# Performance work log

Hardware: AMD Instinct MI355X
Metric: run time of the kernel (lower is better)

The kernel has to match this reference:

```python
import jax, jax.numpy as jnp
import numpy as np

B, SD, VD, AD, E, K = 32768, 96, 512, 12, 8, 2
EPS_LN = 1e-5

def _ln(x, g, b):
    m = x.mean(-1, keepdims=True)
    v = ((x - m) ** 2).mean(-1, keepdims=True)
    return (x - m) / jnp.sqrt(v + EPS_LN) * g + b

def setup_inputs() -> dict:
    key = jax.random.key(0)
    ks = iter(jax.random.split(key, 64))
    def w(shape, s=0.02):
        return jax.random.normal(next(ks), shape, dtype=jnp.float32) * s
    inp = {
        'state_obs': jax.random.normal(next(ks), (B, SD), dtype=jnp.float32),
        'vlm_feature': jax.random.normal(next(ks), (B, VD), dtype=jnp.float32),
        # state encoder (per-expert stacked): 96->256->128, Linear+ELU+LN each
        'sw1': w((E, SD, 256)), 'sb1': jnp.zeros((E, 256)), 'sg1': jnp.ones((E, 256)), 'sh1': jnp.zeros((E, 256)),
        'sw2': w((E, 256, 128)), 'sb2': jnp.zeros((E, 128)), 'sg2': jnp.ones((E, 128)), 'sh2': jnp.zeros((E, 128)),
        # vlm encoder: 512->512->256
        'vw1': w((E, VD, 512)), 'vb1': jnp.zeros((E, 512)), 'vg1': jnp.ones((E, 512)), 'vh1': jnp.zeros((E, 512)),
        'vw2': w((E, 512, 256)), 'vb2': jnp.zeros((E, 256)), 'vg2': jnp.ones((E, 256)), 'vh2': jnp.zeros((E, 256)),
        # fusion: (128+256)=384 -> 512 -> 256 -> 12 (act+LN except last)
        'fw1': w((E, 384, 512)), 'fb1': jnp.zeros((E, 512)), 'fg1': jnp.ones((E, 512)), 'fh1': jnp.zeros((E, 512)),
        'fw2': w((E, 512, 256)), 'fb2': jnp.zeros((E, 256)), 'fg2': jnp.ones((E, 256)), 'fh2': jnp.zeros((E, 256)),
        'fw3': w((E, 256, AD)), 'fb3': jnp.zeros((E, AD)),
        # gate: (96+512)=608 -> 256 -> 128 -> 8, act between hidden layers only
        'gw1': w((SD + VD, 256)), 'gb1': jnp.zeros((256,)),
        'gw2': w((256, 128)), 'gb2': jnp.zeros((128,)),
        'gw3': w((128, E)), 'gb3': jnp.zeros((E,)),
        'logstd': jnp.full((AD,), -1.0, dtype=jnp.float32),
    }
    return inp

def reference(state_obs, vlm_feature,
              sw1, sb1, sg1, sh1, sw2, sb2, sg2, sh2,
              vw1, vb1, vg1, vh1, vw2, vb2, vg2, vh2,
              fw1, fb1, fg1, fh1, fw2, fb2, fg2, fh2, fw3, fb3,
              gw1, gb1, gw2, gb2, gw3, gb3, logstd):
    act = jax.nn.elu
    # run ALL experts densely (faithful to the module)
    h = _ln(act(jnp.einsum('bi,eio->beo', state_obs, sw1) + sb1), sg1, sh1)   # [B,E,256]
    obs_feat = _ln(act(jnp.einsum('bei,eio->beo', h, sw2) + sb2), sg2, sh2)   # [B,E,128]
    h = _ln(act(jnp.einsum('bi,eio->beo', vlm_feature, vw1) + vb1), vg1, vh1) # [B,E,512]
    vlm_feat = _ln(act(jnp.einsum('bei,eio->beo', h, vw2) + vb2), vg2, vh2)   # [B,E,256]
    fused = jnp.concatenate([obs_feat, vlm_feat], axis=-1)                     # [B,E,384]
    h = _ln(act(jnp.einsum('bei,eio->beo', fused, fw1) + fb1), fg1, fh1)
    h = _ln(act(jnp.einsum('bei,eio->beo', h, fw2) + fb2), fg2, fh2)
    all_outputs = jnp.einsum('bei,eio->beo', h, fw3) + fb3                     # [B,E,AD]
    # gate
    g = jnp.concatenate([state_obs, vlm_feature], axis=-1)
    g = act(g @ gw1 + gb1)
    g = act(g @ gw2 + gb2)
    gate_logits = g @ gw3 + gb3
    gate_probs = jax.nn.softmax(gate_logits, axis=-1)                          # [B,E]
    top_k_scores, top_k_indices = jax.lax.top_k(gate_probs, K)                 # [B,K]
    selected = jnp.take_along_axis(all_outputs, top_k_indices[:, :, None], axis=1)  # [B,K,AD]
    weights = top_k_scores / (top_k_scores.sum(axis=1, keepdims=True) + 1e-9)
    fused_output = (selected * weights[:, :, None]).sum(axis=1)                # [B,AD]
    # auxiliary load-balancing loss (Switch-style)
    dispatch = jax.nn.one_hot(top_k_indices, E, dtype=gate_probs.dtype).sum(1) # [B,E]
    f = dispatch.mean(0) / K
    P = gate_probs.mean(0)
    aux_loss = E * jnp.sum(f * P)
    action = fused_output  # deterministic path
    return action, aux_loss, top_k_indices, top_k_scores
```

## Files before the change

### kernel.cpp

```cpp
#include <hip/hip_runtime.h>
#include <cstdint>
#include <cstddef>

#define BROWS 32768
#define NEXP 8
#define CAP 10240
#define CAPBLK (CAP / 64)
#define NBLKC (CAPBLK * NEXP)

typedef short bf16x8 __attribute__((ext_vector_type(8)));
typedef float f32x4 __attribute__((ext_vector_type(4)));
typedef float f32x2 __attribute__((ext_vector_type(2)));

__device__ __forceinline__ unsigned short f2b(float f) {
  union { float f; unsigned u; } v; v.f = f;
  unsigned r = (v.u + 0x7fffu + ((v.u >> 16) & 1u)) >> 16;
  return (unsigned short)r;
}
__device__ __forceinline__ float b2f(unsigned short s) {
  union { unsigned u; float f; } v; v.u = ((unsigned)s) << 16; return v.f;
}
__device__ __forceinline__ float fast_elu(float x) {
  return x > 0.f ? x : __expf(x) - 1.f;
}

template<bool TWOSRC>
__device__ __forceinline__ void gate_gemm_body(
    char* ldsraw, int rb, int nb,
    const float* __restrict__ A0, int As0,
    const float* __restrict__ A1, int As1, int Ks,
    const float* __restrict__ W, const float* __restrict__ bias,
    int K, int N, float* __restrict__ Out) {
  float (*At)[132] = (float(*)[132])ldsraw;
  float (*Bs)[132] = (float(*)[132])(ldsraw + 32 * 132 * 4);

  int tid = threadIdx.x;
  int tx = tid & 15, tyg = tid >> 4;
  int arow = tid >> 1, aq = (tid & 1) * 16;
  int brow = tid >> 3, bc = (tid & 7) * 16;

  f32x2 acc[8][4] = {};

  float4 a0, a1, a2, a3, b0, b1, b2, b3;
  {
    const float* arp = (!TWOSRC || aq < Ks)
        ? (A0 + (size_t)(rb + arow) * As0 + aq)
        : (A1 + (size_t)(rb + arow) * As1 + (aq - Ks));
    a0 = *(const float4*)(arp);
    a1 = *(const float4*)(arp + 4);
    a2 = *(const float4*)(arp + 8);
    a3 = *(const float4*)(arp + 12);
    const float* brp = W + (size_t)brow * N + nb + bc;
    b0 = *(const float4*)(brp);
    b1 = *(const float4*)(brp + 4);
    b2 = *(const float4*)(brp + 8);
    b3 = *(const float4*)(brp + 12);
  }

  const int NT = K / 32;
  for (int kt = 0; kt < NT; ++kt) {
    __syncthreads();
    At[aq + 0][arow] = a0.x;  At[aq + 1][arow] = a0.y;
    At[aq + 2][arow] = a0.z;  At[aq + 3][arow] = a0.w;
    At[aq + 4][arow] = a1.x;  At[aq + 5][arow] = a1.y;
    At[aq + 6][arow] = a1.z;  At[aq + 7][arow] = a1.w;
    At[aq + 8][arow] = a2.x;  At[aq + 9][arow] = a2.y;
    At[aq + 10][arow] = a2.z; At[aq + 11][arow] = a2.w;
    At[aq + 12][arow] = a3.x; At[aq + 13][arow] = a3.y;
    At[aq + 14][arow] = a3.z; At[aq + 15][arow] = a3.w;
    *(float4*)(&Bs[brow][bc])      = b0;
    *(float4*)(&Bs[brow][bc + 4])  = b1;
    *(float4*)(&Bs[brow][bc + 8])  = b2;
    *(float4*)(&Bs[brow][bc + 12]) = b3;
    __syncthreads();

    if (kt + 1 < NT) {
      int ka = (kt + 1) * 32 + aq;
      const float* arp = (!TWOSRC || ka < Ks)
          ? (A0 + (size_t)(rb + arow) * As0 + ka)
          : (A1 + (size_t)(rb + arow) * As1 + (ka - Ks));
      a0 = *(const float4*)(arp);
      a1 = *(const float4*)(arp + 4);
      a2 = *(const float4*)(arp + 8);
      a3 = *(const float4*)(arp + 12);
      const float* brp = W + (size_t)((kt + 1) * 32 + brow) * N + nb + bc;
      b0 = *(const float4*)(brp);
      b1 = *(const float4*)(brp + 4);
      b2 = *(const float4*)(brp + 8);
      b3 = *(const float4*)(brp + 12);
    }

#pragma unroll 4
    for (int kk = 0; kk < 32; ++kk) {
      float4 av0 = *(const float4*)(&At[kk][tyg * 8]);
      float4 av1 = *(const float4*)(&At[kk][tyg * 8 + 4]);
      float4 bq0 = *(const float4*)(&Bs[kk][tx * 8]);
      float4 bq1 = *(const float4*)(&Bs[kk][tx * 8 + 4]);
      f32x2 bp0 = {bq0.x, bq0.y}, bp1 = {bq0.z, bq0.w};
      f32x2 bp2 = {bq1.x, bq1.y}, bp3 = {bq1.z, bq1.w};
      float av[8] = {av0.x, av0.y, av0.z, av0.w, av1.x, av1.y, av1.z, av1.w};
#pragma unroll
      for (int i = 0; i < 8; ++i) {
        f32x2 as = {av[i], av[i]};
        acc[i][0] = __builtin_elementwise_fma(as, bp0, acc[i][0]);
        acc[i][1] = __builtin_elementwise_fma(as, bp1, acc[i][1]);
        acc[i][2] = __builtin_elementwise_fma(as, bp2, acc[i][2]);
        acc[i][3] = __builtin_elementwise_fma(as, bp3, acc[i][3]);
      }
    }
  }

  float4 bia0 = *(const float4*)(&bias[nb + tx * 8]);
  float4 bia1 = *(const float4*)(&bias[nb + tx * 8 + 4]);
  float bia[8] = {bia0.x, bia0.y, bia0.z, bia0.w, bia1.x, bia1.y, bia1.z, bia1.w};

#pragma unroll
  for (int i = 0; i < 8; ++i) {
    float o[8];
#pragma unroll
    for (int j = 0; j < 4; ++j) {
      o[2 * j]     = acc[i][j][0] + bia[2 * j];
      o[2 * j + 1] = acc[i][j][1] + bia[2 * j + 1];
    }
#pragma unroll
    for (int j = 0; j < 8; ++j) o[j] = (o[j] > 0.f) ? o[j] : expm1f(o[j]);
    size_t orow = (size_t)(rb + tyg * 8 + i) * N + nb + tx * 8;
    float4 w0; w0.x = o[0]; w0.y = o[1]; w0.z = o[2]; w0.w = o[3];
    float4 w1; w1.x = o[4]; w1.y = o[5]; w1.z = o[6]; w1.w = o[7];
    *(float4*)(&Out[orow]) = w0;
    *(float4*)(&Out[orow + 4]) = w1;
  }
}

__launch_bounds__(256, 4)
__global__ void k_front(const float* __restrict__ state, const float* __restrict__ vlm,
                        unsigned short* __restrict__ st_bf, unsigned short* __restrict__ vl_bf,
                        int* __restrict__ cntaux,
                        const float* __restrict__ gw1, const float* __restrict__ gb1,
                        float* __restrict__ gh1,
                        const float* __restrict__ s1w, unsigned short* __restrict__ s1d,
                        const float* __restrict__ s2w, unsigned short* __restrict__ s2d,
                        const float* __restrict__ v1w, unsigned short* __restrict__ v1d,
                        const float* __restrict__ v2w, unsigned short* __restrict__ v2d,
                        const float* __restrict__ f1w, unsigned short* __restrict__ f1d,
                        const float* __restrict__ f2w, unsigned short* __restrict__ f2d) {
  __shared__ char lds[2 * 32 * 132 * 4];
  int bid = blockIdx.x, tid = threadIdx.x;

  if (bid < 512) {
    int rb = (bid & 255) * 128, nb = (bid >> 8) * 128;
    gate_gemm_body<true>(lds, rb, nb, state, 96, vlm, 512, 96,
                         gw1, gb1, 608, 256, gh1);
  } else if (bid < 512 + 6144) {
    float (*tile)[33] = (float(*)[33])lds;
    int b2 = bid - 512;
    int e = b2 / 768, r = b2 % 768;
    const float* src; unsigned short* dst; int K, N, Kpad, nbx;
    if (r < 32)       { src = s1w; dst = s1d; K = 96;  N = 256; Kpad = 128; nbx = 4;  }
    else if (r < 64)  { src = s2w; dst = s2d; K = 256; N = 128; Kpad = 256; nbx = 8;  r -= 32;  }
    else if (r < 320) { src = v1w; dst = v1d; K = 512; N = 512; Kpad = 512; nbx = 16; r -= 64;  }
    else if (r < 448) { src = v2w; dst = v2d; K = 512; N = 256; Kpad = 512; nbx = 16; r -= 320; }
    else if (r < 640) { src = f1w; dst = f1d; K = 384; N = 512; Kpad = 384; nbx = 12; r -= 448; }
    else              { src = f2w; dst = f2d; K = 512; N = 256; Kpad = 512; nbx = 16; r -= 640; }
    int k0 = (r % nbx) * 32, n0 = (r / nbx) * 32;
    int tx = tid & 31, ty = tid >> 5;
    for (int i = 0; i < 32; i += 8) {
      int k = k0 + ty + i;
      tile[ty + i][tx] = (k < K) ? src[((size_t)e * K + k) * N + n0 + tx] : 0.f;
    }
    __syncthreads();
    for (int i = 0; i < 32; i += 8) {
      int n = n0 + ty + i;
      dst[((size_t)e * N + n) * Kpad + k0 + tx] = f2b(tile[tx][ty + i]);
    }
  } else {
    int cid = bid - (512 + 6144);
    if (cid == 0 && tid < 64) cntaux[tid] = 0;
    const int NB1 = (BROWS * 128) / 256;
    if (cid < NB1) {
      int i = cid * 256 + tid;
      int r = i >> 7, c = i & 127;
      st_bf[i] = f2b(c < 96 ? state[(size_t)r * 96 + c] : 0.f);
    } else {
      int i = (cid - NB1) * 256 + tid;
      vl_bf[i] = f2b(vlm[i]);
    }
  }
}

#define ACTION_SZ (32768 * 12)
#define AUX_OFF   ACTION_SZ
#define IDX_OFF   (ACTION_SZ + 1)
#define SCO_OFF   (ACTION_SZ + 1 + 32768 * 2)

__launch_bounds__(256, 2)
__global__ void k_gtail(const float* __restrict__ gh1,
                        const float* __restrict__ gw2, const float* __restrict__ gb2,
                        const float* __restrict__ gw3, const float* __restrict__ gb3,
                        float* __restrict__ out, float* __restrict__ aux,
                        int* __restrict__ bcnt, float* __restrict__ selbuf) {
  __shared__ char lds[71680];
  float (*At)[132] = (float(*)[132])lds;
  float (*Bs)[132] = (float(*)[132])(lds + 32 * 132 * 4);
  float (*ghT)[132] = (float(*)[132])lds;
  float* gw3s = (float*)(lds + 67584);
  __shared__ float sprob[8];

  int tid = threadIdx.x;
  int rb = blockIdx.x * 128;
  int tx = tid & 15, tyg = tid >> 4;
  int arow = tid >> 1, aq = (tid & 1) * 16;
  int brow = tid >> 3, bc = (tid & 7) * 16;
  const int N = 128, K = 256;

  f32x2 acc[8][4] = {};
  float4 a0, a1, a2, a3, b0, b1, b2, b3;
  {
    const float* arp = gh1 + (size_t)(rb + arow) * 256 + aq;
    a0 = *(const float4*)(arp);
    a1 = *(const float4*)(arp + 4);
    a2 = *(const float4*)(arp + 8);
    a3 = *(const float4*)(arp + 12);
    const float* brp = gw2 + (size_t)brow * N + bc;
    b0 = *(const float4*)(brp);
    b1 = *(const float4*)(brp + 4);
    b2 = *(const float4*)(brp + 8);
    b3 = *(const float4*)(brp + 12);
  }
  const int NT = K / 32;
  for (int kt = 0; kt < NT; ++kt) {
    __syncthreads();
    At[aq + 0][arow] = a0.x;  At[aq + 1][arow] = a0.y;
    At[aq + 2][arow] = a0.z;  At[aq + 3][arow] = a0.w;
    At[aq + 4][arow] = a1.x;  At[aq + 5][arow] = a1.y;
    At[aq + 6][arow] = a1.z;  At[aq + 7][arow] = a1.w;
    At[aq + 8][arow] = a2.x;  At[aq + 9][arow] = a2.y;
    At[aq + 10][arow] = a2.z; At[aq + 11][arow] = a2.w;
    At[aq + 12][arow] = a3.x; At[aq + 13][arow] = a3.y;
    At[aq + 14][arow] = a3.z; At[aq + 15][arow] = a3.w;
    *(float4*)(&Bs[brow][bc])      = b0;
    *(float4*)(&Bs[brow][bc + 4])  = b1;
    *(float4*)(&Bs[brow][bc + 8])  = b2;
    *(float4*)(&Bs[brow][bc + 12]) = b3;
    __syncthreads();

    if (kt + 1 < NT) {
      int ka = (kt + 1) * 32 + aq;
      const float* arp = gh1 + (size_t)(rb + arow) * 256 + ka;
      a0 = *(const float4*)(arp);
      a1 = *(const float4*)(arp + 4);
      a2 = *(const float4*)(arp + 8);
      a3 = *(const float4*)(arp + 12);
      const float* brp = gw2 + (size_t)((kt + 1) * 32 + brow) * N + bc;
      b0 = *(const float4*)(brp);
      b1 = *(const float4*)(brp + 4);
      b2 = *(const float4*)(brp + 8);
      b3 = *(const float4*)(brp + 12);
    }

#pragma unroll 4
    for (int kk = 0; kk < 32; ++kk) {
      float4 av0 = *(const float4*)(&At[kk][tyg * 8]);
      float4 av1 = *(const float4*)(&At[kk][tyg * 8 + 4]);
      float4 bq0 = *(const float4*)(&Bs[kk][tx * 8]);
      float4 bq1 = *(const float4*)(&Bs[kk][tx * 8 + 4]);
      f32x2 bp0 = {bq0.x, bq0.y}, bp1 = {bq0.z, bq0.w};
      f32x2 bp2 = {bq1.x, bq1.y}, bp3 = {bq1.z, bq1.w};
      float av[8] = {av0.x, av0.y, av0.z, av0.w, av1.x, av1.y, av1.z, av1.w};
#pragma unroll
      for (int i = 0; i < 8; ++i) {
// ... 51 lines not shown
    int i0 = 0, i1;
    float v0 = -1e30f;
#pragma unroll
    for (int j = 0; j < 8; ++j) if (probs[j] > v0) { v0 = probs[j]; i0 = j; }
    float v1 = -1e30f; i1 = (i0 == 0) ? 1 : 0;
#pragma unroll
    for (int j = 0; j < 8; ++j) if (j != i0 && probs[j] > v1) { v1 = probs[j]; i1 = j; }
    float wsum = v0 + v1 + 1e-9f;
    float w0 = v0 / wsum, w1 = v1 / wsum;

    out[IDX_OFF + (size_t)b * 2 + 0] = (float)i0;
    out[IDX_OFF + (size_t)b * 2 + 1] = (float)i1;
    out[SCO_OFF + (size_t)b * 2 + 0] = v0;
    out[SCO_OFF + (size_t)b * 2 + 1] = v1;
    selbuf[(size_t)b * 4 + 0] = (float)i0;
    selbuf[(size_t)b * 4 + 1] = (float)i1;
    selbuf[(size_t)b * 4 + 2] = w0;
    selbuf[(size_t)b * 4 + 3] = w1;

#pragma unroll
    for (int e2 = 0; e2 < 8; ++e2) {
      unsigned long long mm = __ballot(i0 == e2) | __ballot(i1 == e2);
      if (lane == 0) bcnt[((size_t)blockIdx.x * 2 + w) * 8 + e2] = __popcll(mm);
    }
#pragma unroll
    for (int j = 0; j < 8; ++j) {
      float p = probs[j];
#pragma unroll
      for (int mk = 1; mk <= 32; mk <<= 1) p += __shfl_xor(p, mk, 64);
      if (lane == 0) atomicAdd(&sprob[j], p);
    }
  }
  __syncthreads();
  if (tid < 8) atomicAdd(&aux[tid], sprob[tid]);
}

__global__ void k_scanaux(const int* __restrict__ bcnt, int* __restrict__ bbase,
                          int* __restrict__ cnt, const float* __restrict__ aux,
                          float* __restrict__ out) {
  __shared__ int psum[8][8];
  __shared__ int scnt[8];
  int tid = threadIdx.x;
  int e2 = tid & 7, seg = tid >> 3;
  int s = 0;
  for (int i = 0; i < 64; ++i) s += bcnt[(seg * 64 + i) * 8 + e2];
  psum[seg][e2] = s;
  __syncthreads();
  int base = 0;
  for (int t = 0; t < seg; ++t) base += psum[t][e2];
  int run = base;
  for (int i = 0; i < 64; ++i) {
    bbase[(seg * 64 + i) * 8 + e2] = run;
    run += bcnt[(seg * 64 + i) * 8 + e2];
  }
  if (seg == 7) { cnt[e2] = run; scnt[e2] = run; }
  __syncthreads();
  if (tid == 0) {
    float ss = 0.f;
#pragma unroll
    for (int e = 0; e < 8; ++e)
      ss += ((float)scnt[e] / 65536.f) * (aux[e] / 32768.f);
    out[AUX_OFF] = 8.f * ss;
  }
}

__global__ void k_fill(const float* __restrict__ selbuf, const int* __restrict__ bbase,
                       int* __restrict__ perm) {
  int gidx = blockIdx.x;
  int lane = threadIdx.x;
  int b = gidx * 64 + lane;
  int i0 = (int)selbuf[(size_t)b * 4 + 0];
  int i1 = (int)selbuf[(size_t)b * 4 + 1];
  unsigned long long lt = (1ull << lane) - 1ull;
#pragma unroll
  for (int e2 = 0; e2 < 8; ++e2) {
    unsigned long long mm = __ballot(i0 == e2) | __ballot(i1 == e2);
    if (i0 == e2 || i1 == e2) {
      int s = bbase[gidx * 8 + e2] + (int)__popcll(mm & lt);
      if (s < CAP) perm[e2 * CAP + s] = b;
    }
  }
}

template<int K1, int N1, int N2, bool GATHER, bool FCHAIN>
__device__ __forceinline__ void chain_body(
    int bid, char* ldsraw,
    const unsigned short* __restrict__ A, int As,
    const int* __restrict__ perm, const int* __restrict__ cnt,
    const unsigned short* __restrict__ W1, const float* __restrict__ b1v,
    const float* __restrict__ g1v, const float* __restrict__ h1v,
    const unsigned short* __restrict__ W2, const float* __restrict__ b2v,
    const float* __restrict__ g2v, const float* __restrict__ h2v,
    unsigned short* __restrict__ Out, int Os, int Ocol,
    const float* __restrict__ fw3, const float* __restrict__ fb3,
    float* __restrict__ allout) {
  constexpr int WC1 = N1 / 8, NF1 = WC1 / 16;
  constexpr int WC2 = N2 / 8, NF2 = WC2 / 16;
  constexpr int NK1 = K1 / 64;
  constexpr int NS1 = NK1 * 2, NS2 = (N1 / 64) * 2;
  constexpr int PAN = (K1 > N1) ? K1 : N1;
  constexpr int NCH = N2 / 128;
  static_assert(NF1 >= 1 && NF2 >= 1 && K1 % 64 == 0 && N1 % 128 == 0, "shape");

  unsigned short* smP = (unsigned short*)ldsraw;
  float (*red)[8][2] = (float(*)[8][2])(ldsraw + (size_t)64 * PAN * 2);
  float (*rowstat)[2] = (float(*)[2])(ldsraw + (size_t)64 * PAN * 2 + 4096);

  int e = bid & 7;
  int count = cnt[e]; if (count > CAP) count = CAP;
  int rb = (bid >> 3) * 64;
  if (rb >= count) return;

  int tid = threadIdx.x;
  int lane = tid & 63, wn = tid >> 6;
  int l15 = lane & 15, g = lane >> 4;

  {
    int srow = tid >> 3, schunk = tid & 7;
    int slot = rb + srow;
    size_t arow;
    if (GATHER) {
      int s = slot < count ? slot : count - 1;
      arow = (size_t)perm[e * CAP + s];
    } else {
      arow = (size_t)e * CAP + slot;
    }
    const unsigned short* aptr = A + arow * As + schunk * 8;
    int lws = srow * K1 + ((schunk ^ (srow & 7)) << 3);
    uint4 stg[NK1];
#pragma unroll
    for (int kt = 0; kt < NK1; ++kt) stg[kt] = *(const uint4*)(aptr + kt * 64);
#pragma unroll
    for (int kt = 0; kt < NK1; ++kt) *(uint4*)(&smP[lws + kt * 64]) = stg[kt];
  }

  const unsigned short* W1e = W1 + (size_t)e * N1 * K1;
  const unsigned short* bp1[NF1];
#pragma unroll
  for (int nf = 0; nf < NF1; ++nf)
    bp1[nf] = W1e + (size_t)(wn * WC1 + nf * 16 + l15) * K1 + g * 8;

  f32x4 acc1[4][NF1] = {};
  bf16x8 qA[NF1], qB[NF1];
#pragma unroll
  for (int nf = 0; nf < NF1; ++nf) qA[nf] = *(const bf16x8*)(bp1[nf]);
  if (NS1 > 1) {
#pragma unroll
    for (int nf = 0; nf < NF1; ++nf) qB[nf] = *(const bf16x8*)(bp1[nf] + 32);
  }

  __syncthreads();

#pragma unroll
  for (int ks = 0; ks < NS1; ++ks) {
    const int kt = ks >> 1, kk = ks & 1;
    bf16x8 a4[4];
#pragma unroll
    for (int mf = 0; mf < 4; ++mf) {
      int row = mf * 16 + l15;
      int chunk = (kk * 4 + g) ^ (row & 7);
      a4[mf] = *(const bf16x8*)(&smP[row * K1 + kt * 64 + chunk * 8]);
    }
    if ((ks & 1) == 0) {
#pragma unroll
      for (int mf = 0; mf < 4; ++mf)
#pragma unroll
        for (int nf = 0; nf < NF1; ++nf)
          acc1[mf][nf] = __builtin_amdgcn_mfma_f32_16x16x32_bf16(a4[mf], qA[nf], acc1[mf][nf], 0, 0, 0);
      if (ks + 2 < NS1) {
#pragma unroll
        for (int nf = 0; nf < NF1; ++nf) qA[nf] = *(const bf16x8*)(bp1[nf] + (ks + 2) * 32);
      }
    } else {
#pragma unroll
      for (int mf = 0; mf < 4; ++mf)
#pragma unroll
        for (int nf = 0; nf < NF1; ++nf)
          acc1[mf][nf] = __builtin_amdgcn_mfma_f32_16x16x32_bf16(a4[mf], qB[nf], acc1[mf][nf], 0, 0, 0);
      if (ks + 2 < NS1) {
#pragma unroll
        for (int nf = 0; nf < NF1; ++nf) qB[nf] = *(const bf16x8*)(bp1[nf] + (ks + 2) * 32);
      }
    }
  }

  {
    float bia[NF1], gam[NF1], bet[NF1];
#pragma unroll
    for (int nf = 0; nf < NF1; ++nf) {
      int n = wn * WC1 + nf * 16 + l15;
      bia[nf] = b1v[e * N1 + n]; gam[nf] = g1v[e * N1 + n]; bet[nf] = h1v[e * N1 + n];
    }
#pragma unroll
    for (int mf = 0; mf < 4; ++mf)
#pragma unroll
      for (int nf = 0; nf < NF1; ++nf)
#pragma unroll
        for (int r = 0; r < 4; ++r)
          acc1[mf][nf][r] = fast_elu(acc1[mf][nf][r] + bia[nf]);
#pragma unroll
    for (int mf = 0; mf < 4; ++mf)
#pragma unroll
      for (int r = 0; r < 4; ++r) {
        float s1 = 0.f, s2 = 0.f;
#pragma unroll
        for (int nf = 0; nf < NF1; ++nf) {
          float x = acc1[mf][nf][r];
          s1 += x; s2 += x * x;
        }
#pragma unroll
        for (int mk = 1; mk <= 8; mk <<= 1) {
          s1 += __shfl_xor(s1, mk, 64);
          s2 += __shfl_xor(s2, mk, 64);
        }
        if (l15 == 0) {
          int row = mf * 16 + g * 4 + r;
          red[row][wn][0] = s1;
          red[row][wn][1] = s2;
        }
      }
    __syncthreads();
    if (tid < 64) {
      float s1 = 0.f, s2 = 0.f;
#pragma unroll
      for (int j = 0; j < 8; ++j) { s1 += red[tid][j][0]; s2 += red[tid][j][1]; }
      float mean = s1 / (float)N1;
      float var = s2 / (float)N1 - mean * mean;
      rowstat[tid][0] = mean;
      rowstat[tid][1] = rsqrtf(var + 1e-5f);
    }
    __syncthreads();
#pragma unroll
    for (int mf = 0; mf < 4; ++mf)
#pragma unroll
      for (int r = 0; r < 4; ++r) {
        int row = mf * 16 + g * 4 + r;
        float mean = rowstat[row][0], rstd = rowstat[row][1];
#pragma unroll
        for (int nf = 0; nf < NF1; ++nf) {
          int col = wn * WC1 + nf * 16 + l15;
          float y = (acc1[mf][nf][r] - mean) * rstd * gam[nf] + bet[nf];
          int pos = (col & ~63) + ((((col >> 3) & 7) ^ (row & 7)) << 3) + (col & 7);
          smP[row * N1 + pos] = f2b(y);
        }
      }
  }

  const unsigned short* W2e = W2 + (size_t)e * N2 * N1;
  const unsigned short* bp2[NF2];
#pragma unroll
  for (int nf = 0; nf < NF2; ++nf)
    bp2[nf] = W2e + (size_t)(wn * WC2 + nf * 16 + l15) * N1 + g * 8;

  f32x4 acc2[4][NF2] = {};
  bf16x8 pA[NF2], pB[NF2];
#pragma unroll
  for (int nf = 0; nf < NF2; ++nf) pA[nf] = *(const bf16x8*)(bp2[nf]);
  if (NS2 > 1) {
#pragma unroll
    for (int nf = 0; nf < NF2; ++nf) pB[nf] = *(const bf16x8*)(bp2[nf] + 32);
  }

  __syncthreads();

#pragma unroll
  for (int ks = 0; ks < NS2; ++ks) {
    const int kt = ks >> 1, kk = ks & 1;
    bf16x8 a4[4];
#pragma unroll
    for (int mf = 0; mf < 4; ++mf) {
      int row = mf * 16 + l15;
      int chunk = (kk * 4 + g) ^ (row & 7);
      a4[mf] = *(const bf16x8*)(&smP[row * N1 + kt * 64 + chunk * 8]);
    }
    if ((ks & 1) == 0) {
#pragma unroll
      for (int mf = 0; mf < 4; ++mf)
#pragma unroll
        for (int nf = 0; nf < NF2; ++nf)
          acc2[mf][nf] = __builtin_amdgcn_mfma_f32_16x16x32_bf16(a4[mf], pA[nf], acc2[mf][nf], 0, 0, 0);
      if (ks + 2 < NS2) {
#pragma unroll
        for (int nf = 0; nf < NF2; ++nf) pA[nf] = *(const bf16x8*)(bp2[nf] + (ks + 2) * 32);
      }
    } else {
#pragma unroll
      for (int mf = 0; mf < 4; ++mf)
#pragma unroll
        for (int nf = 0; nf < NF2; ++nf)
          acc2[mf][nf] = __builtin_amdgcn_mfma_f32_16x16x32_bf16(a4[mf], pB[nf], acc2[mf][nf], 0, 0, 0);
      if (ks + 2 < NS2) {
#pragma unroll
        for (int nf = 0; nf < NF2; ++nf) pB[nf] = *(const bf16x8*)(bp2[nf] + (ks + 2) * 32);
      }
    }
  }

  {
    float bia[NF2], gam[NF2], bet[NF2];
#pragma unroll
    for (int nf = 0; nf < NF2; ++nf) {
      int n = wn * WC2 + nf * 16 + l15;
      bia[nf] = b2v[e * N2 + n]; gam[nf] = g2v[e * N2 + n]; bet[nf] = h2v[e * N2 + n];
    }
#pragma unroll
    for (int mf = 0; mf < 4; ++mf)
#pragma unroll
      for (int nf = 0; nf < NF2; ++nf)
#pragma unroll
        for (int r = 0; r < 4; ++r)
          acc2[mf][nf][r] = fast_elu(acc2[mf][nf][r] + bia[nf]);
#pragma unroll
    for (int mf = 0; mf < 4; ++mf)
#pragma unroll
      for (int r = 0; r < 4; ++r) {
        float s1 = 0.f, s2 = 0.f;
#pragma unroll
        for (int nf = 0; nf < NF2; ++nf) {
          float x = acc2[mf][nf][r];
          s1 += x; s2 += x * x;
        }
#pragma unroll
        for (int mk = 1; mk <= 8; mk <<= 1) {
          s1 += __shfl_xor(s1, mk, 64);
          s2 += __shfl_xor(s2, mk, 64);
        }
        if (l15 == 0) {
          int row = mf * 16 + g * 4 + r;
          red[row][wn][0] = s1;
          red[row][wn][1] = s2;
        }
      }
    __syncthreads();
    if (tid < 64) {
      float s1 = 0.f, s2 = 0.f;
#pragma unroll
      for (int j = 0; j < 8; ++j) { s1 += red[tid][j][0]; s2 += red[tid][j][1]; }
      float mean = s1 / (float)N2;
      float var = s2 / (float)N2 - mean * mean;
      rowstat[tid][0] = mean;
      rowstat[tid][1] = rsqrtf(var + 1e-5f);
    }
    __syncthreads();
#pragma unroll
    for (int mf = 0; mf < 4; ++mf)
#pragma unroll
      for (int r = 0; r < 4; ++r) {
        int row = mf * 16 + g * 4 + r;
        float mean = rowstat[row][0], rstd = rowstat[row][1];
#pragma unroll
        for (int nf = 0; nf < NF2; ++nf)
          acc2[mf][nf][r] = (acc2[mf][nf][r] - mean) * rstd * gam[nf] + bet[nf];
      }
  }

  if constexpr (!FCHAIN) {
    unsigned short* sm16 = &smP[0];
    int wq = (wn * WC2) >> 7;
    for (int q = 0; q < NCH; ++q) {
      __syncthreads();
      if (NCH == 1 || wq == q) {
#pragma unroll
        for (int mf = 0; mf < 4; ++mf)
#pragma unroll
          for (int r = 0; r < 4; ++r) {
            int row = mf * 16 + g * 4 + r;
            int s = row & 7;
#pragma unroll
            for (int nf = 0; nf < NF2; ++nf) {
              int lc = (wn * WC2 + nf * 16 + l15) - q * 128;
              if (NCH == 1 || (lc >= 0 && lc < 128)) {
                int pos = (((lc >> 3) ^ s) << 3) | (lc & 7);
                sm16[row * 128 + pos] = f2b(acc2[mf][nf][r]);
              }
            }
          }
      }
      __syncthreads();
#pragma unroll
      for (int i = 0; i < 2; ++i) {
        int t = tid + i * 512;
        int row = t >> 4, cc = t & 15;
        int oc = cc ^ (row & 7);
        uint4 v = *(const uint4*)(&sm16[row * 128 + cc * 8]);
        *(uint4*)(&Out[((size_t)e * CAP + rb + row) * Os + Ocol + q * 128 + oc * 8]) = v;
      }
    }
  } else {
    __syncthreads();
    constexpr int H2S = 264;
    float* wsh = (float*)(&smP[64 * H2S]);
#pragma unroll
    for (int mf = 0; mf < 4; ++mf)
#pragma unroll
      for (int r = 0; r < 4; ++r) {
        int row = mf * 16 + g * 4 + r;
#pragma unroll
        for (int nf = 0; nf < NF2; ++nf) {
          int col = wn * WC2 + nf * 16 + l15;
          smP[row * H2S + col] = f2b(acc2[mf][nf][r]);
        }
      }
    for (int i = tid; i < 256 * 12; i += 512) wsh[i] = fw3[(size_t)e * 256 * 12 + i];
    __syncthreads();
#pragma unroll
    for (int it = 0; it < 2; ++it) {
      int idx = tid + it * 512;
      if (idx < 768) {
        int row = idx / 12, j = idx - row * 12;
        int slot2 = rb + row;
        if (slot2 < count) {
          float a = fb3[e * 12 + j];
          for (int c = 0; c < 256; ++c)
            a += b2f(smP[row * H2S + c]) * wsh[c * 12 + j];
          int arow = perm[e * CAP + slot2];
          allout[((size_t)arow * 8 + e) * 12 + j] = a;
        }
      }
    }
  }
}

__launch_bounds__(512, 4)
__global__ void k_sv(const unsigned short* __restrict__ st_bf,
                     const unsigned short* __restrict__ vl_bf,
                     const int* __restrict__ perm, const int* __restrict__ cnt,
                     const unsigned short* __restrict__ wS1, const float* __restrict__ sb1,
                     const float* __restrict__ sg1, const float* __restrict__ sh1,
                     const unsigned short* __restrict__ wS2, const float* __restrict__ sb2,
                     const float* __restrict__ sg2, const float* __restrict__ sh2,
                     const unsigned short* __restrict__ wV1, const float* __restrict__ vb1,
                     const float* __restrict__ vg1, const float* __restrict__ vh1,
                     const unsigned short* __restrict__ wV2, const float* __restrict__ vb2,
                     const float* __restrict__ vg2, const float* __restrict__ vh2,
                     unsigned short* __restrict__ bufF) {
  __shared__ char lds[70144];
  int bid = blockIdx.x;
  if (bid < NBLKC) {
    chain_body<512, 512, 256, true, false>(bid, lds, vl_bf, 512, perm, cnt,
        wV1, vb1, vg1, vh1, wV2, vb2, vg2, vh2,
        bufF, 384, 128, nullptr, nullptr, nullptr);
  } else {
    chain_body<128, 256, 128, true, false>(bid - NBLKC, lds, st_bf, 128, perm, cnt,
        wS1, sb1, sg1, sh1, wS2, sb2, sg2, sh2,
        bufF, 384, 0, nullptr, nullptr, nullptr);
  }
}

__launch_bounds__(512, 4)
__global__ void k_chainF(const unsigned short* __restrict__ bufF,
                         const int* __restrict__ perm, const int* __restrict__ cnt,
                         const unsigned short* __restrict__ wF1, const float* __restrict__ fb1,
                         const float* __restrict__ fg1, const float* __restrict__ fh1,
                         const unsigned short* __restrict__ wF2, const float* __restrict__ fb2,
                         const float* __restrict__ fg2, const float* __restrict__ fh2,
                         const float* __restrict__ fw3, const float* __restrict__ fb3,
                         float* __restrict__ allout) {
  __shared__ char lds[70144];
  chain_body<384, 512, 256, false, true>(blockIdx.x, lds, bufF, 384, perm, cnt,
      wF1, fb1, fg1, fh1, wF2, fb2, fg2, fh2,
      nullptr, 0, 0, fw3, fb3, allout);
}

__global__ void k_mix(const float* __restrict__ selbuf, const float* __restrict__ allout,
                      float* __restrict__ out) {
  int b = blockIdx.x * 256 + threadIdx.x;
  int i0 = (int)selbuf[(size_t)b * 4 + 0];
  int i1 = (int)selbuf[(size_t)b * 4 + 1];
  float w0 = selbuf[(size_t)b * 4 + 2];
  float w1 = selbuf[(size_t)b * 4 + 3];
  const float* a0 = allout + ((size_t)b * 8 + i0) * 12;
  const float* a1 = allout + ((size_t)b * 8 + i1) * 12;
#pragma unroll
  for (int j = 0; j < 12; ++j)
    out[(size_t)b * 12 + j] = w0 * a0[j] + w1 * a1[j];
}


extern "C" void kernel_launch(void* const* d_in, const int* in_sizes, int n_in,
                              void* d_out, int out_size, void* d_ws, size_t ws_size,
                              hipStream_t stream) {
  const float* state = (const float*)d_in[0];
  const float* vlm   = (const float*)d_in[1];
  const float* sw1 = (const float*)d_in[2];  const float* sb1 = (const float*)d_in[3];
  const float* sg1 = (const float*)d_in[4];  const float* sh1 = (const float*)d_in[5];
  const float* sw2 = (const float*)d_in[6];  const float* sb2 = (const float*)d_in[7];
  const float* sg2 = (const float*)d_in[8];  const float* sh2 = (const float*)d_in[9];
  const float* vw1 = (const float*)d_in[10]; const float* vb1 = (const float*)d_in[11];
  const float* vg1 = (const float*)d_in[12]; const float* vh1 = (const float*)d_in[13];
  const float* vw2 = (const float*)d_in[14]; const float* vb2 = (const float*)d_in[15];
  const float* vg2 = (const float*)d_in[16]; const float* vh2 = (const float*)d_in[17];
  const float* fw1 = (const float*)d_in[18]; const float* fb1 = (const float*)d_in[19];
  const float* fg1 = (const float*)d_in[20]; const float* fh1 = (const float*)d_in[21];
  const float* fw2 = (const float*)d_in[22]; const float* fb2 = (const float*)d_in[23];
  const float* fg2 = (const float*)d_in[24]; const float* fh2 = (const float*)d_in[25];
  const float* fw3 = (const float*)d_in[26]; const float* fb3 = (const float*)d_in[27];
  const float* gw1 = (const float*)d_in[28]; const float* gb1 = (const float*)d_in[29];
  const float* gw2 = (const float*)d_in[30]; const float* gb2 = (const float*)d_in[31];
  const float* gw3 = (const float*)d_in[32]; const float* gb3 = (const float*)d_in[33];

  char* ws = (char*)d_ws;
  size_t off = 0;
  auto alloc = [&](size_t bytes) -> char* {
    char* p = ws + off;
    off = (off + bytes + 255) & ~(size_t)255;
    return p;
  };
  unsigned short* st_bf = (unsigned short*)alloc((size_t)BROWS * 128 * 2);
  unsigned short* vl_bf = (unsigned short*)alloc((size_t)BROWS * 512 * 2);
  unsigned short* bufF  = (unsigned short*)alloc((size_t)NEXP * CAP * 384 * 2);
  float* allout = (float*)alloc((size_t)BROWS * 8 * 12 * 4);
  float* gh1    = (float*)alloc((size_t)BROWS * 256 * 4);
  float* selbuf = (float*)alloc((size_t)BROWS * 4 * 4);
  int*   perm   = (int*)alloc((size_t)NEXP * CAP * 4);
  int*   bcnt   = (int*)alloc(512 * 8 * 4);
  int*   bbase  = (int*)alloc(512 * 8 * 4);
  char*  cntaux = alloc(256);
  int*   cnt = (int*)cntaux;
  float* aux = (float*)(cntaux + 64);
  unsigned short* wt_s1 = (unsigned short*)alloc((size_t)8 * 256 * 128 * 2);
  unsigned short* wt_s2 = (unsigned short*)alloc((size_t)8 * 128 * 256 * 2);
  unsigned short* wt_v1 = (unsigned short*)alloc((size_t)8 * 512 * 512 * 2);
  unsigned short* wt_v2 = (unsigned short*)alloc((size_t)8 * 256 * 512 * 2);
  unsigned short* wt_f1 = (unsigned short*)alloc((size_t)8 * 512 * 384 * 2);
  unsigned short* wt_f2 = (unsigned short*)alloc((size_t)8 * 256 * 512 * 2);
  (void)ws_size; (void)in_sizes; (void)n_in; (void)out_size;

  float* outf = (float*)d_out;

  const int NBCV = (BROWS * 128) / 256 + (BROWS * 512) / 256;
  k_front<<<512 + 6144 + NBCV, 256, 0, stream>>>(
      state, vlm, st_bf, vl_bf, (int*)cntaux, gw1, gb1, gh1,
      sw1, wt_s1, sw2, wt_s2, vw1, wt_v1, vw2, wt_v2, fw1, wt_f1, fw2, wt_f2);

  k_gtail<<<256, 256, 0, stream>>>(gh1, gw2, gb2, gw3, gb3, outf, aux, bcnt, selbuf);
  k_scanaux<<<1, 64, 0, stream>>>(bcnt, bbase, cnt, aux, outf);
  k_fill<<<512, 64, 0, stream>>>(selbuf, bbase, perm);

  k_sv<<<2 * NBLKC, 512, 0, stream>>>(st_bf, vl_bf, perm, cnt,
      wt_s1, sb1, sg1, sh1, wt_s2, sb2, sg2, sh2,
      wt_v1, vb1, vg1, vh1, wt_v2, vb2, vg2, vh2, bufF);
  k_chainF<<<NBLKC, 512, 0, stream>>>(bufF, perm, cnt,
      wt_f1, fb1, fg1, fh1, wt_f2, fb2, fg2, fh2, fw3, fb3, allout);

  k_mix<<<BROWS / 256, 256, 0, stream>>>(selbuf, allout, outf);
}
```

Before: 535.2 us.

## Fuse state, VLM and fusion expert chains into one LDS-resident kernel

Merges the k_sv and k_chainF kernels into a single k_chain kernel. Each 64-row tile now runs the VLM encoder, the state encoder and the fusion MLP back to back, keeping the intermediate 384-wide fused activations in LDS. This removes the bufF global round trip and one kernel launch. In exchange, the state and VLM encoders for a tile now run serially in one block instead of as parallel blocks, which halves the grid for that stage and lengthens each block.

Measured after the change: 662.3 us. 1.24x slower.

```diff
diff --git a/kernel.cpp b/kernel.cpp
--- a/kernel.cpp
+++ b/kernel.cpp
@@ -403,72 +403,59 @@
   }
 }
 
-template<int K1, int N1, int N2, bool GATHER, bool FCHAIN>
-__device__ __forceinline__ void chain_body(
-    int bid, char* ldsraw,
-    const unsigned short* __restrict__ A, int As,
-    const int* __restrict__ perm, const int* __restrict__ cnt,
+
+template<int K1, int ABASE>
+__device__ __forceinline__ void stage_panel(
+    unsigned short* smP, const unsigned short* __restrict__ A, int As,
+    const int* __restrict__ perm, int e, int rb, int count, int tid) {
+  constexpr int NK1 = K1 / 64;
+  int srow = tid >> 3, schunk = tid & 7;
+  int slot = rb + srow;
+  int s = slot < count ? slot : count - 1;
+  size_t arow = (size_t)perm[e * CAP + s];
+  const unsigned short* aptr = A + arow * As + schunk * 8;
+  int lws = ABASE + srow * K1 + ((schunk ^ (srow & 7)) << 3);
+  uint4 stg[NK1];
+#pragma unroll
+  for (int kt = 0; kt < NK1; ++kt) stg[kt] = *(const uint4*)(aptr + kt * 64);
+#pragma unroll
+  for (int kt = 0; kt < NK1; ++kt) *(uint4*)(&smP[lws + kt * 64]) = stg[kt];
+}
+
+template<int K1, int N1, int N2, int ABASE, int HBASE, bool MIXED>
+__device__ __forceinline__ void gemm2_ln(
+    unsigned short* smP, float (*red)[8][2], float (*rowstat)[2],
+    int e, int tid,
     const unsigned short* __restrict__ W1, const float* __restrict__ b1v,
     const float* __restrict__ g1v, const float* __restrict__ h1v,
     const unsigned short* __restrict__ W2, const float* __restrict__ b2v,
     const float* __restrict__ g2v, const float* __restrict__ h2v,
-    unsigned short* __restrict__ Out, int Os, int Ocol,
-    const float* __restrict__ fw3, const float* __restrict__ fb3,
-    float* __restrict__ allout) {
+    f32x4 (&acc2)[4][N2 / 128]) {
   constexpr int WC1 = N1 / 8, NF1 = WC1 / 16;
   constexpr int WC2 = N2 / 8, NF2 = WC2 / 16;
-  constexpr int NK1 = K1 / 64;
-  constexpr int NS1 = NK1 * 2, NS2 = (N1 / 64) * 2;
-  constexpr int PAN = (K1 > N1) ? K1 : N1;
-  constexpr int NCH = N2 / 128;
-  static_assert(NF1 >= 1 && NF2 >= 1 && K1 % 64 == 0 && N1 % 128 == 0, "shape");
-
-  unsigned short* smP = (unsigned short*)ldsraw;
-  float (*red)[8][2] = (float(*)[8][2])(ldsraw + (size_t)64 * PAN * 2);
-  float (*rowstat)[2] = (float(*)[2])(ldsraw + (size_t)64 * PAN * 2 + 4096);
-
-  int e = bid & 7;
-  int count = cnt[e]; if (count > CAP) count = CAP;
-  int rb = (bid >> 3) * 64;
-  if (rb >= count) return;
-
-  int tid = threadIdx.x;
+  constexpr int NS1 = (K1 / 64) * 2, NS2 = (N1 / 64) * 2;
   int lane = tid & 63, wn = tid >> 6;
   int l15 = lane & 15, g = lane >> 4;
 
-  {
-    int srow = tid >> 3, schunk = tid & 7;
-    int slot = rb + srow;
-    size_t arow;
-    if (GATHER) {
-      int s = slot < count ? slot : count - 1;
-      arow = (size_t)perm[e * CAP + s];
-    } else {
-      arow = (size_t)e * CAP + slot;
-    }
-    const unsigned short* aptr = A + arow * As + schunk * 8;
-    int lws = srow * K1 + ((schunk ^ (srow & 7)) << 3);
-    uint4 stg[NK1];
-#pragma unroll
-    for (int kt = 0; kt < NK1; ++kt) stg[kt] = *(const uint4*)(aptr + kt * 64);
-#pragma unroll
-    for (int kt = 0; kt < NK1; ++kt) *(uint4*)(&smP[lws + kt * 64]) = stg[kt];
-  }
-
   const unsigned short* W1e = W1 + (size_t)e * N1 * K1;
   const unsigned short* bp1[NF1];
 #pragma unroll
   for (int nf = 0; nf < NF1; ++nf)
     bp1[nf] = W1e + (size_t)(wn * WC1 + nf * 16 + l15) * K1 + g * 8;
 
-  f32x4 acc1[4][NF1] = {};
+  f32x4 acc1[4][NF1];
+  {
+    f32x4 z = {0.f, 0.f, 0.f, 0.f};
+#pragma unroll
+    for (int mf = 0; mf < 4; ++mf)
+#pragma unroll
+      for (int nf = 0; nf < NF1; ++nf) acc1[mf][nf] = z;
+  }
   bf16x8 qA[NF1], qB[NF1];
 #pragma unroll
   for (int nf = 0; nf < NF1; ++nf) qA[nf] = *(const bf16x8*)(bp1[nf]);
-  if (NS1 > 1) {
-#pragma unroll
-    for (int nf = 0; nf < NF1; ++nf) qB[nf] = *(const bf16x8*)(bp1[nf] + 32);
-  }
+#pragma unroll
+  for (int nf = 0; nf < NF1; ++nf) qB[nf] = *(const bf16x8*)(bp1[nf] + 32);
 
   __syncthreads();
 
@@ -480,7 +467,13 @@
     for (int mf = 0; mf < 4; ++mf) {
       int row = mf * 16 + l15;
       int chunk = (kk * 4 + g) ^ (row & 7);
-      a4[mf] = *(const bf16x8*)(&smP[row * K1 + kt * 64 + chunk * 8]);
+      if constexpr (MIXED) {
+        a4[mf] = (kt < 2)
+            ? *(const bf16x8*)(&smP[16384 + row * 128 + kt * 64 + chunk * 8])
+            : *(const bf16x8*)(&smP[row * 256 + (kt - 2) * 64 + chunk * 8]);
+      } else {
+        a4[mf] = *(const bf16x8*)(&smP[ABASE + row * K1 + kt * 64 + chunk * 8]);
+      }
     }
     if ((ks & 1) == 0) {
 #pragma unroll
@@ -562,7 +555,7 @@
           int col = wn * WC1 + nf * 16 + l15;
           float y = (acc1[mf][nf][r] - mean) * rstd * gam[nf] + bet[nf];
           int pos = (col & ~63) + ((((col >> 3) & 7) ^ (row & 7)) << 3) + (col & 7);
-          smP[row * N1 + pos] = f2b(y);
+          smP[HBASE + row * N1 + pos] = f2b(y);
         }
       }
   }
@@ -573,14 +566,18 @@
   for (int nf = 0; nf < NF2; ++nf)
     bp2[nf] = W2e + (size_t)(wn * WC2 + nf * 16 + l15) * N1 + g * 8;
 
-  f32x4 acc2[4][NF2] = {};
+  {
+    f32x4 z = {0.f, 0.f, 0.f, 0.f};
+#pragma unroll
+    for (int mf = 0; mf < 4; ++mf)
+#pragma unroll
+      for (int nf = 0; nf < NF2; ++nf) acc2[mf][nf] = z;
+  }
   bf16x8 pA[NF2], pB[NF2];
 #pragma unroll
   for (int nf = 0; nf < NF2; ++nf) pA[nf] = *(const bf16x8*)(bp2[nf]);
-  if (NS2 > 1) {
-#pragma unroll
-    for (int nf = 0; nf < NF2; ++nf) pB[nf] = *(const bf16x8*)(bp2[nf] + 32);
-  }
+#pragma unroll
+  for (int nf = 0; nf < NF2; ++nf) pB[nf] = *(const bf16x8*)(bp2[nf] + 32);
 
   __syncthreads();
 
@@ -592,7 +589,7 @@
     for (int mf = 0; mf < 4; ++mf) {
       int row = mf * 16 + l15;
       int chunk = (kk * 4 + g) ^ (row & 7);
-      a4[mf] = *(const bf16x8*)(&smP[row * N1 + kt * 64 + chunk * 8]);
+      a4[mf] = *(const bf16x8*)(&smP[HBASE + row * N1 + kt * 64 + chunk * 8]);
     }
     if ((ks & 1) == 0) {
 #pragma unroll
@@ -674,52 +671,92 @@
           acc2[mf][nf][r] = (acc2[mf][nf][r] - mean) * rstd * gam[nf] + bet[nf];
       }
   }
-
-  if constexpr (!FCHAIN) {
-    unsigned short* sm16 = &smP[0];
-    int wq = (wn * WC2) >> 7;
-    for (int q = 0; q < NCH; ++q) {
-      __syncthreads();
-      if (NCH == 1 || wq == q) {
-#pragma unroll
-        for (int mf = 0; mf < 4; ++mf)
-#pragma unroll
-          for (int r = 0; r < 4; ++r) {
-            int row = mf * 16 + g * 4 + r;
-            int s = row & 7;
-#pragma unroll
-            for (int nf = 0; nf < NF2; ++nf) {
-              int lc = (wn * WC2 + nf * 16 + l15) - q * 128;
-              if (NCH == 1 || (lc >= 0 && lc < 128)) {
-                int pos = (((lc >> 3) ^ s) << 3) | (lc & 7);
-                sm16[row * 128 + pos] = f2b(acc2[mf][nf][r]);
-              }
-            }
-          }
-      }
-      __syncthreads();
-#pragma unroll
-      for (int i = 0; i < 2; ++i) {
-        int t = tid + i * 512;
-        int row = t >> 4, cc = t & 15;
-        int oc = cc ^ (row & 7);
-        uint4 v = *(const uint4*)(&sm16[row * 128 + cc * 8]);
-        *(uint4*)(&Out[((size_t)e * CAP + rb + row) * Os + Ocol + q * 128 + oc * 8]) = v;
-      }
-    }
-  } else {
-    __syncthreads();
+}
+
+template<int N2, int OUTBASE>
+__device__ __forceinline__ void write_out(unsigned short* smP, int tid,
+                                          f32x4 (&acc2)[4][N2 / 128]) {
+  constexpr int WC2 = N2 / 8, NF2 = N2 / 128;
+  int lane = tid & 63, wn = tid >> 6;
+  int l15 = lane & 15, g = lane >> 4;
+#pragma unroll
+  for (int mf = 0; mf < 4; ++mf)
+#pragma unroll
+    for (int r = 0; r < 4; ++r) {
+      int row = mf * 16 + g * 4 + r;
+#pragma unroll
+      for (int nf = 0; nf < NF2; ++nf) {
+        int col = wn * WC2 + nf * 16 + l15;
+        int pos = (col & ~63) + ((((col >> 3) & 7) ^ (row & 7)) << 3) + (col & 7);
+        smP[OUTBASE + row * N2 + pos] = f2b(acc2[mf][nf][r]);
+      }
+    }
+}
+
+__launch_bounds__(512, 4)
+__global__ void k_chain(const unsigned short* __restrict__ st_bf,
+                        const unsigned short* __restrict__ vl_bf,
+                        const int* __restrict__ perm, const int* __restrict__ cnt,
+                        const unsigned short* __restrict__ wS1, const float* __restrict__ sb1,
+                        const float* __restrict__ sg1, const float* __restrict__ sh1,
+                        const unsigned short* __restrict__ wS2, const float* __restrict__ sb2,
+                        const float* __restrict__ sg2, const float* __restrict__ sh2,
+                        const unsigned short* __restrict__ wV1, const float* __restrict__ vb1,
+                        const float* __restrict__ vg1, const float* __restrict__ vh1,
+                        const unsigned short* __restrict__ wV2, const float* __restrict__ vb2,
+                        const float* __restrict__ vg2, const float* __restrict__ vh2,
+                        const unsigned short* __restrict__ wF1, const float* __restrict__ fb1,
+                        const float* __restrict__ fg1, const float* __restrict__ fh1,
+                        const unsigned short* __restrict__ wF2, const float* __restrict__ fb2,
+                        const float* __restrict__ fg2, const float* __restrict__ fh2,
+                        const float* __restrict__ fw3, const float* __restrict__ fb3,
+                        float* __restrict__ allout) {
+  __shared__ char lds[70144];
+  unsigned short* smP = (unsigned short*)lds;
+  float (*red)[8][2] = (float(*)[8][2])(lds + 65536);
+  float (*rowstat)[2] = (float(*)[2])(lds + 65536 + 4096);
+
+  int bid = blockIdx.x, tid = threadIdx.x;
+  int e = bid & 7;
+  int count = cnt[e]; if (count > CAP) count = CAP;
+  int rb = (bid >> 3) * 64;
+  if (rb >= count) return;
+
+  stage_panel<512, 0>(smP, vl_bf, 512, perm, e, rb, count, tid);
+  {
+    f32x4 acc2v[4][2];
+    gemm2_ln<512, 512, 256, 0, 0, false>(smP, red, rowstat, e, tid,
+        wV1, vb1, vg1, vh1, wV2, vb2, vg2, vh2, acc2v);
+    write_out<256, 0>(smP, tid, acc2v);
+  }
+
+  stage_panel<128, 16384>(smP, st_bf, 128, perm, e, rb, count, tid);
+  {
+    f32x4 acc2s[4][1];
+    gemm2_ln<128, 256, 128, 16384, 16384, false>(smP, red, rowstat, e, tid,
+        wS1, sb1, sg1, sh1, wS2, sb2, sg2, sh2, acc2s);
+    write_out<128, 16384>(smP, tid, acc2s);
+  }
+
+  f32x4 acc2f[4][2];
+  gemm2_ln<384, 512, 256, 0, 0, true>(smP, red, rowstat, e, tid,
+      wF1, fb1, fg1, fh1, wF2, fb2, fg2, fh2, acc2f);
+
+  __syncthreads();
+  {
     constexpr int H2S = 264;
     float* wsh = (float*)(&smP[64 * H2S]);
+    int lane = tid & 63, wn = tid >> 6;
+    int l15 = lane & 15, g = lane >> 4;
 #pragma unroll
     for (int mf = 0; mf < 4; ++mf)
 #pragma unroll
       for (int r = 0; r < 4; ++r) {
         int row = mf * 16 + g * 4 + r;
 #pragma unroll
-        for (int nf = 0; nf < NF2; ++nf) {
-          int col = wn * WC2 + nf * 16 + l15;
-          smP[row * H2S + col] = f2b(acc2[mf][nf][r]);
+        for (int nf = 0; nf < 2; ++nf) {
+          int col = wn * 32 + nf * 16 + l15;
+          smP[row * H2S + col] = f2b(acc2f[mf][nf][r]);
         }
       }
     for (int i = tid; i < 256 * 12; i += 512) wsh[i] = fw3[(size_t)e * 256 * 12 + i];
@@ -740,47 +777,6 @@
       }
     }
   }
-}
-
-__launch_bounds__(512, 4)
-__global__ void k_sv(const unsigned short* __restrict__ st_bf,
-                     const unsigned short* __restrict__ vl_bf,
-                     const int* __restrict__ perm, const int* __restrict__ cnt,
-                     const unsigned short* __restrict__ wS1, const float* __restrict__ sb1,
-                     const float* __restrict__ sg1, const float* __restrict__ sh1,
-                     const unsigned short* __restrict__ wS2, const float* __restrict__ sb2,
-                     const float* __restrict__ sg2, const float* __restrict__ sh2,
-                     const unsigned short* __restrict__ wV1, const float* __restrict__ vb1,
-                     const float* __restrict__ vg1, const float* __restrict__ vh1,
-                     const unsigned short* __restrict__ wV2, const float* __restrict__ vb2,
-                     const float* __restrict__ vg2, const float* __restrict__ vh2,
-                     unsigned short* __restrict__ bufF) {
-  __shared__ char lds[70144];
-  int bid = blockIdx.x;
-  if (bid < NBLKC) {
-    chain_body<512, 512, 256, true, false>(bid, lds, vl_bf, 512, perm, cnt,
-        wV1, vb1, vg1, vh1, wV2, vb2, vg2, vh2,
-        bufF, 384, 128, nullptr, nullptr, nullptr);
-  } else {
-    chain_body<128, 256, 128, true, false>(bid - NBLKC, lds, st_bf, 128, perm, cnt,
-        wS1, sb1, sg1, sh1, wS2, sb2, sg2, sh2,
-        bufF, 384, 0, nullptr, nullptr, nullptr);
-  }
-}
-
-__launch_bounds__(512, 4)
-__global__ void k_chainF(const unsigned short* __restrict__ bufF,
-                         const int* __restrict__ perm, const int* __restrict__ cnt,
-                         const unsigned short* __restrict__ wF1, const float* __restrict__ fb1,
-                         const float* __restrict__ fg1, const float* __restrict__ fh1,
-                         const unsigned short* __restrict__ wF2, const float* __restrict__ fb2,
-                         const float* __restrict__ fg2, const float* __restrict__ fh2,
-                         const float* __restrict__ fw3, const float* __restrict__ fb3,
-                         float* __restrict__ allout) {
-  __shared__ char lds[70144];
-  chain_body<384, 512, 256, false, true>(blockIdx.x, lds, bufF, 384, perm, cnt,
-      wF1, fb1, fg1, fh1, wF2, fb2, fg2, fh2,
-      nullptr, 0, 0, fw3, fb3, allout);
 }
 
 __global__ void k_mix(const float* __restrict__ selbuf, const float* __restrict__ allout,
@@ -829,7 +825,6 @@
   };
   unsigned short* st_bf = (unsigned short*)alloc((size_t)BROWS * 128 * 2);
   unsigned short* vl_bf = (unsigned short*)alloc((size_t)BROWS * 512 * 2);
-  unsigned short* bufF  = (unsigned short*)alloc((size_t)NEXP * CAP * 384 * 2);
   float* allout = (float*)alloc((size_t)BROWS * 8 * 12 * 4);
   float* gh1    = (float*)alloc((size_t)BROWS * 256 * 4);
   float* selbuf = (float*)alloc((size_t)BROWS * 4 * 4);
@@ -858,10 +853,9 @@
   k_scanaux<<<1, 64, 0, stream>>>(bcnt, bbase, cnt, aux, outf);
   k_fill<<<512, 64, 0, stream>>>(selbuf, bbase, perm);
 
-  k_sv<<<2 * NBLKC, 512, 0, stream>>>(st_bf, vl_bf, perm, cnt,
+  k_chain<<<NBLKC, 512, 0, stream>>>(st_bf, vl_bf, perm, cnt,
       wt_s1, sb1, sg1, sh1, wt_s2, sb2, sg2, sh2,
-      wt_v1, vb1, vg1, vh1, wt_v2, vb2, vg2, vh2, bufF);
-  k_chainF<<<NBLKC, 512, 0, stream>>>(bufF, perm, cnt,
+      wt_v1, vb1, vg1, vh1, wt_v2, vb2, vg2, vh2,
       wt_f1, fb1, fg1, fh1, wt_f2, fb2, fg2, fh2, fw3, fb3, allout);
 
   k_mix<<<BROWS / 256, 256, 0, stream>>>(selbuf, allout, outf);
```

## Split gate first-layer GEMM along K and combine partials in a new kernel

Applied to the files above, without the earlier changes.

The first gate GEMM (608->256) now runs as a split-K computation: 1024 blocks instead of 512, each covering about half of the K tiles and writing raw partial sums to two scratch buffers. A new elementwise kernel adds the two partials plus the bias and applies ELU to produce gh1. The aim is more parallelism and shorter per-block K loops in the front kernel. The cost is two extra 32 MB fp32 scratch writes and reads plus an additional kernel launch.

After: 610.0 us. +14.0%, slower.

```diff
diff --git a/kernel.cpp b/kernel.cpp
--- a/kernel.cpp
+++ b/kernel.cpp
@@ -24,13 +24,13 @@
   return x > 0.f ? x : __expf(x) - 1.f;
 }
 
-template<bool TWOSRC>
+template<bool TWOSRC, bool RAW>
 __device__ __forceinline__ void gate_gemm_body(
-    char* ldsraw, int rb, int nb,
+    char* ldsraw, int rb, int nb, int ktb, int ntk,
     const float* __restrict__ A0, int As0,
     const float* __restrict__ A1, int As1, int Ks,
     const float* __restrict__ W, const float* __restrict__ bias,
-    int K, int N, float* __restrict__ Out) {
+    int N, float* __restrict__ Out) {
   float (*At)[132] = (float(*)[132])ldsraw;
   float (*Bs)[132] = (float(*)[132])(ldsraw + 32 * 132 * 4);
 
@@ -43,22 +43,23 @@
 
   float4 a0, a1, a2, a3, b0, b1, b2, b3;
   {
-    const float* arp = (!TWOSRC || aq < Ks)
-        ? (A0 + (size_t)(rb + arow) * As0 + aq)
-        : (A1 + (size_t)(rb + arow) * As1 + (aq - Ks));
+    int ka = ktb * 32 + aq;
+    const float* arp = (!TWOSRC || ka < Ks)
+        ? (A0 + (size_t)(rb + arow) * As0 + ka)
+        : (A1 + (size_t)(rb + arow) * As1 + (ka - Ks));
     a0 = *(const float4*)(arp);
     a1 = *(const float4*)(arp + 4);
     a2 = *(const float4*)(arp + 8);
     a3 = *(const float4*)(arp + 12);
-    const float* brp = W + (size_t)brow * N + nb + bc;
+    const float* brp = W + (size_t)(ktb * 32 + brow) * N + nb + bc;
     b0 = *(const float4*)(brp);
     b1 = *(const float4*)(brp + 4);
     b2 = *(const float4*)(brp + 8);
     b3 = *(const float4*)(brp + 12);
   }
 
-  const int NT = K / 32;
-  for (int kt = 0; kt < NT; ++kt) {
+  const int ke = ktb + ntk;
+  for (int kt = ktb; kt < ke; ++kt) {
     __syncthreads();
     At[aq + 0][arow] = a0.x;  At[aq + 1][arow] = a0.y;
     At[aq + 2][arow] = a0.z;  At[aq + 3][arow] = a0.w;
@@ -74,7 +75,7 @@
     *(float4*)(&Bs[brow][bc + 12]) = b3;
     __syncthreads();
 
-    if (kt + 1 < NT) {
+    if (kt + 1 < ke) {
       int ka = (kt + 1) * 32 + aq;
       const float* arp = (!TWOSRC || ka < Ks)
           ? (A0 + (size_t)(rb + arow) * As0 + ka)
@@ -110,6 +111,20 @@
     }
   }
 
+  if (RAW) {
+#pragma unroll
+    for (int i = 0; i < 8; ++i) {
+      size_t orow = (size_t)(rb + tyg * 8 + i) * N + nb + tx * 8;
+      float4 w0; w0.x = acc[i][0][0]; w0.y = acc[i][0][1];
+      w0.z = acc[i][1][0]; w0.w = acc[i][1][1];
+      float4 w1; w1.x = acc[i][2][0]; w1.y = acc[i][2][1];
+      w1.z = acc[i][3][0]; w1.w = acc[i][3][1];
+      *(float4*)(&Out[orow]) = w0;
+      *(float4*)(&Out[orow + 4]) = w1;
+    }
+    return;
+  }
+
   float4 bia0 = *(const float4*)(&bias[nb + tx * 8]);
   float4 bia1 = *(const float4*)(&bias[nb + tx * 8 + 4]);
   float bia[8] = {bia0.x, bia0.y, bia0.z, bia0.w, bia1.x, bia1.y, bia1.z, bia1.w};
@@ -136,8 +151,8 @@
 __global__ void k_front(const float* __restrict__ state, const float* __restrict__ vlm,
                         unsigned short* __restrict__ st_bf, unsigned short* __restrict__ vl_bf,
                         int* __restrict__ cntaux,
-                        const float* __restrict__ gw1, const float* __restrict__ gb1,
-                        float* __restrict__ gh1,
+                        const float* __restrict__ gw1,
+                        float* __restrict__ gh1a, float* __restrict__ gh1b,
                         const float* __restrict__ s1w, unsigned short* __restrict__ s1d,
                         const float* __restrict__ s2w, unsigned short* __restrict__ s2d,
                         const float* __restrict__ v1w, unsigned short* __restrict__ v1d,
@@ -147,13 +162,19 @@
   __shared__ char lds[2 * 32 * 132 * 4];
   int bid = blockIdx.x, tid = threadIdx.x;
 
-  if (bid < 512) {
-    int rb = (bid & 255) * 128, nb = (bid >> 8) * 128;
-    gate_gemm_body<true>(lds, rb, nb, state, 96, vlm, 512, 96,
-                         gw1, gb1, 608, 256, gh1);
-  } else if (bid < 512 + 6144) {
+  if (bid < 1024) {
+    int rb = (bid & 255) * 128;
+    int nb = ((bid >> 8) & 1) * 128;
+    int z  = bid >> 9;
+    if (z == 0)
+      gate_gemm_body<true, true>(lds, rb, nb, 0, 10, state, 96, vlm, 512, 96,
+                                 gw1, nullptr, 256, gh1a);
+    else
+      gate_gemm_body<true, true>(lds, rb, nb, 10, 9, state, 96, vlm, 512, 96,
+                                 gw1, nullptr, 256, gh1b);
+  } else if (bid < 1024 + 6144) {
     float (*tile)[33] = (float(*)[33])lds;
-    int b2 = bid - 512;
+    int b2 = bid - 1024;
     int e = b2 / 768, r = b2 % 768;
     const float* src; unsigned short* dst; int K, N, Kpad, nbx;
     if (r < 32)       { src = s1w; dst = s1d; K = 96;  N = 256; Kpad = 128; nbx = 4;  }
@@ -174,7 +195,7 @@
       dst[((size_t)e * N + n) * Kpad + k0 + tx] = f2b(tile[tx][ty + i]);
     }
   } else {
-    int cid = bid - (512 + 6144);
+    int cid = bid - (1024 + 6144);
     if (cid == 0 && tid < 64) cntaux[tid] = 0;
     const int NB1 = (BROWS * 128) / 256;
     if (cid < NB1) {
@@ -186,6 +207,29 @@
       vl_bf[i] = f2b(vlm[i]);
     }
   }
+}
+
+__global__ void k_comb(const float* __restrict__ a, const float* __restrict__ b,
+                       const float* __restrict__ gb1, float* __restrict__ out) {
+  int i = (blockIdx.x * 256 + threadIdx.x) * 8;
+  int col = i & 255;
+  float4 x0 = *(const float4*)(&a[i]);
+  float4 x1 = *(const float4*)(&a[i + 4]);
+  float4 y0 = *(const float4*)(&b[i]);
+  float4 y1 = *(const float4*)(&b[i + 4]);
+  float4 c0 = *(const float4*)(&gb1[col]);
+  float4 c1 = *(const float4*)(&gb1[col + 4]);
+  float o[8];
+  o[0] = x0.x + y0.x + c0.x; o[1] = x0.y + y0.y + c0.y;
+  o[2] = x0.z + y0.z + c0.z; o[3] = x0.w + y0.w + c0.w;
+  o[4] = x1.x + y1.x + c1.x; o[5] = x1.y + y1.y + c1.y;
+  o[6] = x1.z + y1.z + c1.z; o[7] = x1.w + y1.w + c1.w;
+#pragma unroll
+  for (int j = 0; j < 8; ++j) o[j] = (o[j] > 0.f) ? o[j] : expm1f(o[j]);
+  float4 w0; w0.x = o[0]; w0.y = o[1]; w0.z = o[2]; w0.w = o[3];
+  float4 w1; w1.x = o[4]; w1.y = o[5]; w1.z = o[6]; w1.w = o[7];
+  *(float4*)(&out[i]) = w0;
+  *(float4*)(&out[i + 4]) = w1;
 }
 
 #define ACTION_SZ (32768 * 12)
@@ -831,6 +875,8 @@
   unsigned short* vl_bf = (unsigned short*)alloc((size_t)BROWS * 512 * 2);
   unsigned short* bufF  = (unsigned short*)alloc((size_t)NEXP * CAP * 384 * 2);
   float* allout = (float*)alloc((size_t)BROWS * 8 * 12 * 4);
+  float* gh1a   = (float*)alloc((size_t)BROWS * 256 * 4);
+  float* gh1b   = (float*)alloc((size_t)BROWS * 256 * 4);
   float* gh1    = (float*)alloc((size_t)BROWS * 256 * 4);
   float* selbuf = (float*)alloc((size_t)BROWS * 4 * 4);
   int*   perm   = (int*)alloc((size_t)NEXP * CAP * 4);
@@ -850,10 +896,11 @@
   float* outf = (float*)d_out;
 
   const int NBCV = (BROWS * 128) / 256 + (BROWS * 512) / 256;
-  k_front<<<512 + 6144 + NBCV, 256, 0, stream>>>(
-      state, vlm, st_bf, vl_bf, (int*)cntaux, gw1, gb1, gh1,
+  k_front<<<1024 + 6144 + NBCV, 256, 0, stream>>>(
+      state, vlm, st_bf, vl_bf, (int*)cntaux, gw1, gh1a, gh1b,
       sw1, wt_s1, sw2, wt_s2, vw1, wt_v1, vw2, wt_v2, fw1, wt_f1, fw2, wt_f2);
 
+  k_comb<<<(BROWS * 256) / (256 * 8), 256, 0, stream>>>(gh1a, gh1b, gb1, gh1);
   k_gtail<<<256, 256, 0, stream>>>(gh1, gw2, gb2, gw3, gb3, outf, aux, bcnt, selbuf);
   k_scanaux<<<1, 64, 0, stream>>>(bcnt, bbase, cnt, aux, outf);
   k_fill<<<512, 64, 0, stream>>>(selbuf, bbase, perm);
```
